# Performance work log

Measured on AMD Instinct MI355X. Metric: run time of the kernel, lower is better.

The kernel has to match this reference:

```python
import jax, jax.numpy as jnp
import numpy as np

N = 50000        # nodes
E = 800000       # edges (before self loops)
G = 512          # graphs
H = 2            # heads
FIN = 128        # in_features
CH = 64          # hidden per head
COUT = 32        # out_features
NEG_SLOPE = 0.2  # PyG GATConv default
BN_EPS = 1e-5


def _gat(x, src, dst, W, a_src, a_dst, b, concat, n):
    # x: [n, F], W: [F, H*C], a_src/a_dst: [H, C]
    h = (x @ W).reshape(n, a_src.shape[0], a_src.shape[1])        # [n, H, C]
    e = jax.nn.leaky_relu((h * a_src).sum(-1)[src]
                          + (h * a_dst).sum(-1)[dst], NEG_SLOPE)  # [Etot, H]
    # per-destination segment softmax (self loops guarantee nonempty segments)
    m = jax.ops.segment_max(e, dst, num_segments=n)
    ex = jnp.exp(e - m[dst])
    s = jax.ops.segment_sum(ex, dst, num_segments=n)
    alpha = ex / (s[dst] + 1e-16)                                 # [Etot, H]
    out = jax.ops.segment_sum(h[src] * alpha[:, :, None], dst, num_segments=n)
    out = out.reshape(n, -1) if concat else out.mean(axis=1)
    return out + b


def _bn(x, gamma, beta, mean, var):
    # BatchNorm1d in eval mode (running statistics)
    return (x - mean) * jax.lax.rsqrt(var + BN_EPS) * gamma + beta


def setup_inputs() -> dict:
    key = jax.random.key(0)
    ks = jax.random.split(key, 12)
    x = jax.random.normal(ks[0], (N, FIN), dtype=jnp.float32)
    edge_index = jax.random.randint(ks[1], (2, E), 0, N, dtype=jnp.int32)
    batch = jnp.sort(jax.random.randint(ks[2], (N,), 0, G, dtype=jnp.int32))
    inp = {"x": x, "edge_index": edge_index, "batch": batch}
    # layer 1: GATConv(FIN -> CH, heads=H, concat=True)
    inp["W1"] = jax.random.normal(ks[3], (FIN, H * CH), dtype=jnp.float32) * 0.1
    inp["as1"] = jax.random.normal(ks[4], (H, CH), dtype=jnp.float32) * 0.1
    inp["ad1"] = jax.random.normal(ks[5], (H, CH), dtype=jnp.float32) * 0.1
    inp["b1"] = jnp.zeros((H * CH,), dtype=jnp.float32)
    inp["bn1_gamma"] = jnp.ones((H * CH,), dtype=jnp.float32)
    inp["bn1_beta"] = jnp.zeros((H * CH,), dtype=jnp.float32)
    inp["bn1_mean"] = jax.random.normal(ks[6], (H * CH,), dtype=jnp.float32) * 0.05
    inp["bn1_var"] = jnp.ones((H * CH,), dtype=jnp.float32)
    # layer 2: GATConv(H*CH -> COUT, heads=H, concat=False)
    inp["W2"] = jax.random.normal(ks[7], (H * CH, H * COUT), dtype=jnp.float32) * 0.1
    inp["as2"] = jax.random.normal(ks[8], (H, COUT), dtype=jnp.float32) * 0.1
    inp["ad2"] = jax.random.normal(ks[9], (H, COUT), dtype=jnp.float32) * 0.1
    inp["b2"] = jnp.zeros((COUT,), dtype=jnp.float32)
    inp["bn2_gamma"] = jnp.ones((COUT,), dtype=jnp.float32)
    inp["bn2_beta"] = jnp.zeros((COUT,), dtype=jnp.float32)
    inp["bn2_mean"] = jax.random.normal(ks[10], (COUT,), dtype=jnp.float32) * 0.05
    inp["bn2_var"] = jnp.ones((COUT,), dtype=jnp.float32)
    return inp


def reference(x, edge_index, batch,
              W1, as1, ad1, b1, bn1_gamma, bn1_beta, bn1_mean, bn1_var,
              W2, as2, ad2, b2, bn2_gamma, bn2_beta, bn2_mean, bn2_var):
    n = x.shape[0]
    sl = jnp.arange(n, dtype=edge_index.dtype)
    src = jnp.concatenate([edge_index[0], sl])  # PyG add_self_loops=True
    dst = jnp.concatenate([edge_index[1], sl])
    h = _gat(x, src, dst, W1, as1, ad1, b1, True, n)
    h = jax.nn.relu(_bn(h, bn1_gamma, bn1_beta, bn1_mean, bn1_var))
    h = _gat(h, src, dst, W2, as2, ad2, b2, False, n)
    h = _bn(h, bn2_gamma, bn2_beta, bn2_mean, bn2_var)
    # global mean pool over graphs
    sums = jax.ops.segment_sum(h, batch, num_segments=G)
    cnts = jax.ops.segment_sum(jnp.ones((n,), h.dtype), batch, num_segments=G)
    pooled = sums / jnp.maximum(cnts, 1.0)[:, None]
    return jax.nn.log_softmax(pooled, axis=1)
```

## Files before the change

### kernel.cpp

```cpp
#include <hip/hip_runtime.h>
#include <hip/hip_bf16.h>

#define NEG_SLOPE 0.2f
#define BN_EPS 1e-5f
#define BSHIFT 7
#define P_PART 256
#define MAXB 512

typedef unsigned int uint32;
typedef unsigned short ushort16;
typedef __attribute__((ext_vector_type(8))) short bf16x8;
typedef __attribute__((ext_vector_type(4))) float f32x4;

__device__ __forceinline__ ushort16 f2bf(float f) {
    uint32 u = __float_as_uint(f);
    u = (u + 0x7fff + ((u >> 16) & 1)) >> 16;
    return (ushort16)u;
}
__device__ __forceinline__ float bfu_lo(uint32 u) { return __uint_as_float(u << 16); }
__device__ __forceinline__ float bfu_hi(uint32 u) { return __uint_as_float(u & 0xffff0000u); }

__global__ __launch_bounds__(256) void hist_part(const int* __restrict__ ei, int E, int Etot,
                                                 int nbuck, int chunk, int* __restrict__ hist) {
    const int p = blockIdx.x;
    __shared__ int lh[MAXB];
    for (int i = threadIdx.x; i < nbuck; i += 256) lh[i] = 0;
    __syncthreads();
    const int beg = p * chunk;
    const int end = min(beg + chunk, Etot);
    for (int i = beg + threadIdx.x; i < end; i += 256) {
        int d = (i < E) ? ei[E + i] : i - E;
        atomicAdd(&lh[d >> BSHIFT], 1);
    }
    __syncthreads();
    for (int i = threadIdx.x; i < nbuck; i += 256) hist[(size_t)i * P_PART + p] = lh[i];
}

__global__ __launch_bounds__(P_PART) void row_scan(int* __restrict__ hist,
                                                   int* __restrict__ rowtot) {
    const int b = blockIdx.x;
    __shared__ int s[P_PART];
    const int t = threadIdx.x;
    int v = hist[(size_t)b * P_PART + t];
    s[t] = v;
    __syncthreads();
    for (int off = 1; off < P_PART; off <<= 1) {
        int u = (t >= off) ? s[t - off] : 0;
        __syncthreads();
        s[t] += u;
        __syncthreads();
    }
    hist[(size_t)b * P_PART + t] = s[t] - v;
    if (t == P_PART - 1) rowtot[b] = s[t];
}

__global__ __launch_bounds__(512) void tot_scan(const int* __restrict__ rowtot,
                                                int* __restrict__ bbase, int nbuck, int Etot) {
    __shared__ int s[512];
    const int t = threadIdx.x;
    int v = (t < nbuck) ? rowtot[t] : 0;
    s[t] = v;
    __syncthreads();
    for (int off = 1; off < 512; off <<= 1) {
        int u = (t >= off) ? s[t - off] : 0;
        __syncthreads();
        s[t] += u;
        __syncthreads();
    }
    if (t < nbuck) bbase[t] = s[t] - v;
    if (t == 0) bbase[nbuck] = Etot;
}

__global__ __launch_bounds__(256) void rank_scatter(const int* __restrict__ ei, int E, int Etot,
                                                    int nbuck, int chunk,
                                                    const int* __restrict__ hist,
                                                    const int* __restrict__ bbase,
                                                    uint32* __restrict__ ebuf) {
    const int p = blockIdx.x;
    __shared__ int cur[MAXB];
    for (int i = threadIdx.x; i < nbuck; i += 256)
        cur[i] = bbase[i] + hist[(size_t)i * P_PART + p];
    __syncthreads();
    const int beg = p * chunk;
    const int end = min(beg + chunk, Etot);
    for (int i = beg + threadIdx.x; i < end; i += 256) {
        int s_, d_;
        if (i < E) { s_ = ei[i]; d_ = ei[E + i]; }
        else       { s_ = d_ = i - E; }
        int pos = atomicAdd(&cur[d_ >> BSHIFT], 1);
        ebuf[pos] = ((uint32)(d_ & ((1 << BSHIFT) - 1)) << 25) | (uint32)s_;
    }
}

__global__ __launch_bounds__(256) void bucket_place(
    const int* __restrict__ bbase, const uint32* __restrict__ ebuf, int N,
    int* __restrict__ base, int* __restrict__ csr_src) {
    const int bk = blockIdx.x;
    __shared__ int ldeg[1 << BSHIFT];
    __shared__ int sscan[1 << BSHIFT];
    __shared__ int lcur[1 << BSHIFT];
    const int t = threadIdx.x;
    if (t < (1 << BSHIFT)) { ldeg[t] = 0; lcur[t] = 0; }
    __syncthreads();
    const int beg = bbase[bk], end = bbase[bk + 1];
    for (int i = beg + t; i < end; i += 256) atomicAdd(&ldeg[ebuf[i] >> 25], 1);
    __syncthreads();
    if (t < 128) sscan[t] = ldeg[t];
    __syncthreads();
    for (int off = 1; off < 128; off <<= 1) {
        int v = 0;
        if (t < 128 && t >= off) v = sscan[t - off];
        __syncthreads();
        if (t < 128) sscan[t] += v;
        __syncthreads();
    }
    if (t < 128) {
        int node = (bk << BSHIFT) + t;
        if (node < N) base[node] = beg + sscan[t] - ldeg[t];
    }
    __syncthreads();
    for (int i = beg + t; i < end; i += 256) {
        uint32 pk = ebuf[i];
        int dl = (int)(pk >> 25);
        int s_ = (int)(pk & 0x1FFFFFFu);
        int pos = beg + (sscan[dl] - ldeg[dl]) + atomicAdd(&lcur[dl], 1);
        csr_src[pos] = s_;
    }
}

__global__ void graph_bounds(const int* __restrict__ batch, int N, int G,
                             int* __restrict__ gstart) {
    int g = blockIdx.x * blockDim.x + threadIdx.x;
    if (g > G) return;
    if (g == G) { gstart[G] = N; return; }
    int lo = 0, hi = N;
    while (lo < hi) { int mid = (lo + hi) >> 1; if (batch[mid] < g) lo = mid + 1; else hi = mid; }
    gstart[g] = lo;
}

template <int OC, int C>
__global__ void pack_w(const float* __restrict__ W, const float* __restrict__ a_s,
                       const float* __restrict__ a_d, ushort16* __restrict__ wt) {
    const int col = blockIdx.x;
    const int k = threadIdx.x;
    float v = 0.f;
    if (col < OC) {
        v = W[k * OC + col];
    } else if (col < OC + 2) {
        int hh = col - OC;
        float s = 0.f;
        for (int c = 0; c < C; ++c) s += W[k * OC + hh * C + c] * a_s[hh * C + c];
        v = s;
    } else if (col < OC + 4) {
        int hh = col - OC - 2;
        float s = 0.f;
        for (int c = 0; c < C; ++c) s += W[k * OC + hh * C + c] * a_d[hh * C + c];
        v = s;
    }
    wt[(size_t)col * 128 + k] = f2bf(v);
}

template <int OC, int NT, bool AF32>
__global__ __launch_bounds__(256) void gemm_mfma(
    const void* __restrict__ xin, const ushort16* __restrict__ wt,
    ushort16* __restrict__ h, float4* __restrict__ att, float2* __restrict__ asc, int N) {
    const int wave = threadIdx.x >> 6, lane = threadIdx.x & 63;
    const int tile = blockIdx.x * 4 + wave;
    if (tile * 16 >= N) return;
    const int m = lane & 15, quad = lane >> 4;
    const int node = tile * 16 + m;

    bf16x8 a[4];
    if (AF32) {
        const float* xr = (const float*)xin + (size_t)node * 128 + quad * 8;
#pragma unroll
        for (int c = 0; c < 4; ++c) {
            float4 u = *(const float4*)(xr + c * 32);
            float4 v = *(const float4*)(xr + c * 32 + 4);
            bf16x8 t;
            t[0] = (short)f2bf(u.x); t[1] = (short)f2bf(u.y);
            t[2] = (short)f2bf(u.z); t[3] = (short)f2bf(u.w);
            t[4] = (short)f2bf(v.x); t[5] = (short)f2bf(v.y);
            t[6] = (short)f2bf(v.z); t[7] = (short)f2bf(v.w);
            a[c] = t;
        }
    } else {
        const ushort16* xr = (const ushort16*)xin + (size_t)node * 128 + quad * 8;
#pragma unroll
        for (int c = 0; c < 4; ++c) a[c] = *(const bf16x8*)(xr + c * 32);
    }

    for (int t = 0; t < NT; ++t) {
        const ushort16* wr = wt + ((size_t)(t * 16 + m)) * 128 + quad * 8;
        bf16x8 b[4];
#pragma unroll
        for (int c = 0; c < 4; ++c) b[c] = *(const bf16x8*)(wr + c * 32);
        f32x4 acc = {0.f, 0.f, 0.f, 0.f};
#pragma unroll
        for (int c = 0; c < 4; ++c)
            acc = __builtin_amdgcn_mfma_f32_16x16x32_bf16(a[c], b[c], acc, 0, 0, 0);
        if (t * 16 < OC) {
#pragma unroll
            for (int r = 0; r < 4; ++r) {
                int nrow = tile * 16 + quad * 4 + r;
                h[(size_t)nrow * OC + t * 16 + m] = f2bf(acc[r]);
            }
        } else if (m < 4) {
#pragma unroll
            for (int r = 0; r < 4; ++r) {
                int nrow = tile * 16 + quad * 4 + r;
                ((float*)(att + nrow))[m] = acc[r];
                if (m < 2) ((float*)(asc + nrow))[m] = acc[r];
            }
        }
    }
}

__global__ __launch_bounds__(256) void gat_gather1(
    const int* __restrict__ base, const int* __restrict__ csr_src, int Etot, int N,
    const ushort16* __restrict__ h, const float4* __restrict__ att,
    const float2* __restrict__ asc,
    const float* __restrict__ b, const float* __restrict__ g, const float* __restrict__ be,
    const float* __restrict__ mu, const float* __restrict__ var,
    ushort16* __restrict__ outb) {
    const int node = __builtin_amdgcn_readfirstlane(blockIdx.x * 4 + (threadIdx.x >> 6));
    if (node >= N) return;
    const int t = threadIdx.x & 63;
    const int sub = t >> 4;
    const int q = t & 15;
    const int hh = q >> 3;
    const int beg = base[node];
    const int end = (node + 1 < N) ? base[node + 1] : Etot;
    const int deg = end - beg;
    const float4 adn = att[node];

    float a0 = 0.f, a1 = 0.f, a2 = 0.f, a3 = 0.f;
    float a4 = 0.f, a5 = 0.f, a6 = 0.f, a7 = 0.f;
    float ssum0 = 0.f, ssum1 = 0.f;

    for (int c0e = 0; c0e < deg; c0e += 64) {
        const int rel = c0e + t;
        const bool ok = rel < deg;
        const int sidxme = csr_src[beg + (ok ? rel : 0)];
        const float2 av = asc[sidxme];
        float e0 = av.x + adn.z, e1 = av.y + adn.w;
        e0 = e0 > 0.f ? e0 : NEG_SLOPE * e0;
        e1 = e1 > 0.f ? e1 : NEG_SLOPE * e1;
        const float x0 = ok ? __expf(e0) : 0.f;
        const float x1 = ok ? __expf(e1) : 0.f;
        float r0 = x0, r1 = x1;
#pragma unroll
        for (int off = 1; off < 64; off <<= 1) {
            r0 += __shfl_xor(r0, off, 64);
            r1 += __shfl_xor(r1, off, 64);
        }
        ssum0 += r0;
        ssum1 += r1;
        const int degc = min(deg - c0e, 64);
        const int kkmax = (degc + 3) >> 2;
        for (int kk = 0; kk < kkmax; kk += 4) {
            int sidx[4];
            float exv[4];
            uint4 hv[4];
#pragma unroll
            for (int j = 0; j < 4; ++j) {
                int sl = min(4 * (kk + j) + sub, 63);
                sidx[j] = __shfl(sidxme, sl, 64);
                float f0 = __shfl(x0, sl, 64);
                float f1 = __shfl(x1, sl, 64);
                exv[j] = hh ? f1 : f0;
                hv[j] = *(const uint4*)(h + (size_t)sidx[j] * 128 + 8 * q);
            }
#pragma unroll
            for (int j = 0; j < 4; ++j) {
                const float ex = exv[j];
                a0 += ex * bfu_lo(hv[j].x);
                a1 += ex * bfu_hi(hv[j].x);
                a2 += ex * bfu_lo(hv[j].y);
                a3 += ex * bfu_hi(hv[j].y);
                a4 += ex * bfu_lo(hv[j].z);
                a5 += ex * bfu_hi(hv[j].z);
                a6 += ex * bfu_lo(hv[j].w);
                a7 += ex * bfu_hi(hv[j].w);
            }
        }
    }
#pragma unroll
    for (int off = 16; off <= 32; off <<= 1) {
        a0 += __shfl_xor(a0, off, 64);
        a1 += __shfl_xor(a1, off, 64);
        a2 += __shfl_xor(a2, off, 64);
        a3 += __shfl_xor(a3, off, 64);
        a4 += __shfl_xor(a4, off, 64);
        a5 += __shfl_xor(a5, off, 64);
        a6 += __shfl_xor(a6, off, 64);
        a7 += __shfl_xor(a7, off, 64);
    }
    if (t < 16) {
        const float inv = 1.f / ((hh ? ssum1 : ssum0) + 1e-16f);
        const int c0 = 8 * q;
        float va[8] = {a0, a1, a2, a3, a4, a5, a6, a7};
        uint32 pk[4];
#pragma unroll
        for (int i = 0; i < 8; i += 2) {
            float v0 = va[i] * inv + b[c0 + i];
            float v1 = va[i + 1] * inv + b[c0 + i + 1];
            v0 = fmaxf((v0 - mu[c0 + i]) * rsqrtf(var[c0 + i] + BN_EPS) * g[c0 + i] + be[c0 + i], 0.f);
            v1 = fmaxf((v1 - mu[c0 + i + 1]) * rsqrtf(var[c0 + i + 1] + BN_EPS) * g[c0 + i + 1] + be[c0 + i + 1], 0.f);
            pk[i >> 1] = (uint32)f2bf(v0) | ((uint32)f2bf(v1) << 16);
        }
        uint4 r = make_uint4(pk[0], pk[1], pk[2], pk[3]);
        *(uint4*)(outb + (size_t)node * 128 + c0) = r;
    }
}

__global__ __launch_bounds__(256) void gat_gather2(
    const int* __restrict__ base, const int* __restrict__ csr_src, int Etot, int N,
    const ushort16* __restrict__ h2, const float4* __restrict__ att,
    const float2* __restrict__ asc,
    const float* __restrict__ b2, const float* __restrict__ g, const float* __restrict__ be,
    const float* __restrict__ mu, const float* __restrict__ var,
    float* __restrict__ node_out) {
    const int node = __builtin_amdgcn_readfirstlane(blockIdx.x * 4 + (threadIdx.x >> 6));
    if (node >= N) return;
    const int t = threadIdx.x & 63;
    const int sub = t >> 4;
    const int q = t & 15;
    const int hh = q >> 3;
    const int beg = base[node];
    const int end = (node + 1 < N) ? base[node + 1] : Etot;
    const int deg = end - beg;
    const float4 adn = att[node];

    float a0 = 0.f, a1 = 0.f, a2 = 0.f, a3 = 0.f;
    float ssum0 = 0.f, ssum1 = 0.f;

    for (int c0e = 0; c0e < deg; c0e += 64) {
        const int rel = c0e + t;
        const bool ok = rel < deg;
        const int sidxme = csr_src[beg + (ok ? rel : 0)];
        const float2 av = asc[sidxme];
        float e0 = av.x + adn.z, e1 = av.y + adn.w;
        e0 = e0 > 0.f ? e0 : NEG_SLOPE * e0;
        e1 = e1 > 0.f ? e1 : NEG_SLOPE * e1;
        const float x0 = ok ? __expf(e0) : 0.f;
        const float x1 = ok ? __expf(e1) : 0.f;
        float r0 = x0, r1 = x1;
#pragma unroll
        for (int off = 1; off < 64; off <<= 1) {
            r0 += __shfl_xor(r0, off, 64);
            r1 += __shfl_xor(r1, off, 64);
        }
        ssum0 += r0;
        ssum1 += r1;
        const int degc = min(deg - c0e, 64);
        const int kkmax = (degc + 3) >> 2;
        for (int kk = 0; kk < kkmax; kk += 4) {
            int sidx[4];
            float exv[4];
            uint2 hv[4];
#pragma unroll
            for (int j = 0; j < 4; ++j) {
                int sl = min(4 * (kk + j) + sub, 63);
                sidx[j] = __shfl(sidxme, sl, 64);
                float f0 = __shfl(x0, sl, 64);
                float f1 = __shfl(x1, sl, 64);
                exv[j] = hh ? f1 : f0;
                hv[j] = *(const uint2*)(h2 + (size_t)sidx[j] * 64 + 4 * q);
            }
#pragma unroll
            for (int j = 0; j < 4; ++j) {
                const float ex = exv[j];
                a0 += ex * bfu_lo(hv[j].x);
                a1 += ex * bfu_hi(hv[j].x);
                a2 += ex * bfu_lo(hv[j].y);
                a3 += ex * bfu_hi(hv[j].y);
            }
        }
    }
#pragma unroll
    for (int off = 16; off <= 32; off <<= 1) {
        a0 += __shfl_xor(a0, off, 64);
        a1 += __shfl_xor(a1, off, 64);
        a2 += __shfl_xor(a2, off, 64);
        a3 += __shfl_xor(a3, off, 64);
    }
    const float inv = 1.f / ((hh ? ssum1 : ssum0) + 1e-16f);
    float v0 = a0 * inv, v1 = a1 * inv, v2 = a2 * inv, v3 = a3 * inv;
    const int src = (t & 15) + 8;
    float p0 = __shfl(v0, src, 64);
    float p1 = __shfl(v1, src, 64);
    float p2 = __shfl(v2, src, 64);
    float p3 = __shfl(v3, src, 64);
    if (t < 8) {
        const int c0 = 4 * t;
        float m0 = 0.5f * (v0 + p0) + b2[c0];
        float m1 = 0.5f * (v1 + p1) + b2[c0 + 1];
        float m2 = 0.5f * (v2 + p2) + b2[c0 + 2];
        float m3 = 0.5f * (v3 + p3) + b2[c0 + 3];
        m0 = (m0 - mu[c0]) * rsqrtf(var[c0] + BN_EPS) * g[c0] + be[c0];
        m1 = (m1 - mu[c0 + 1]) * rsqrtf(var[c0 + 1] + BN_EPS) * g[c0 + 1] + be[c0 + 1];
        m2 = (m2 - mu[c0 + 2]) * rsqrtf(var[c0 + 2] + BN_EPS) * g[c0 + 2] + be[c0 + 2];
        m3 = (m3 - mu[c0 + 3]) * rsqrtf(var[c0 + 3] + BN_EPS) * g[c0 + 3] + be[c0 + 3];
        *(float4*)(node_out + (size_t)node * 32 + c0) = make_float4(m0, m1, m2, m3);
    }
}

__global__ __launch_bounds__(256) void pool_logsoftmax(
    const float* __restrict__ node_out, const int* __restrict__ gstart,
    float* __restrict__ out) {
    const int gidx = blockIdx.x;
    const int tid = threadIdx.x;
    const int c = tid & 31, r = tid >> 5;
    const int n0 = gstart[gidx], n1 = gstart[gidx + 1];
    float s = 0.f;
    for (int n = n0 + r; n < n1; n += 8) s += node_out[(size_t)n * 32 + c];
    __shared__ float red[8][32];
    red[r][c] = s;
    __syncthreads();
    if (r == 0) {
        float tot = red[0][c];
#pragma unroll
        for (int k = 1; k < 8; ++k) tot += red[k][c];
        float v = tot / fmaxf((float)(n1 - n0), 1.f);
        float m = v;
#pragma unroll
        for (int off = 16; off >= 1; off >>= 1) m = fmaxf(m, __shfl_xor(m, off, 64));
        float ex = __expf(v - m);
        float ssum = ex;
#pragma unroll
        for (int off = 16; off >= 1; off >>= 1) ssum += __shfl_xor(ssum, off, 64);
        out[gidx * 32 + c] = v - m - logf(ssum);
    }
}

extern "C" void kernel_launch(void* const* d_in, const int* in_sizes, int n_in,
                              void* d_out, int out_size, void* d_ws, size_t ws_size,
                              hipStream_t stream) {
    const float* x   = (const float*)d_in[0];
    const int* ei    = (const int*)d_in[1];
    const int* batch = (const int*)d_in[2];
    const float* W1  = (const float*)d_in[3];
    const float* as1 = (const float*)d_in[4];
    const float* ad1 = (const float*)d_in[5];
    const float* b1  = (const float*)d_in[6];
    const float* g1  = (const float*)d_in[7];
    const float* be1 = (const float*)d_in[8];
    const float* mu1 = (const float*)d_in[9];
    const float* vr1 = (const float*)d_in[10];
    const float* W2  = (const float*)d_in[11];
    const float* as2 = (const float*)d_in[12];
    const float* ad2 = (const float*)d_in[13];
    const float* b2  = (const float*)d_in[14];
    const float* g2  = (const float*)d_in[15];
    const float* be2 = (const float*)d_in[16];
    const float* mu2 = (const float*)d_in[17];
    const float* vr2 = (const float*)d_in[18];
    float* out = (float*)d_out;

    const int N = in_sizes[0] / 128;
    const int E = in_sizes[1] / 2;
    const int Etot = E + N;
    const int G = out_size / 32;
    const int nbuck = (N + (1 << BSHIFT) - 1) >> BSHIFT;
    const int chunk = (Etot + P_PART - 1) / P_PART;
    const int M = nbuck * P_PART;
    const int ntile = (N + 15) / 16;
    const int gemm_grid = (ntile + 3) / 4;

    float* p = (float*)d_ws;
    size_t o = 0;
    auto al = [&]() { o = (o + 3) & ~(size_t)3; };
    ushort16* h1b   = (ushort16*)(p + o); o += (size_t)N * 64;  al();
    ushort16* agg1b = (ushort16*)(p + o); o += (size_t)N * 64;  al();
    ushort16* h2b   = (ushort16*)(p + o); o += (size_t)N * 32;  al();
    float4* att1 = (float4*)(p + o); o += (size_t)N * 4;  al();
    float4* att2 = (float4*)(p + o); o += (size_t)N * 4;  al();
    float2* asc1 = (float2*)(p + o); o += (size_t)N * 2;  al();
    float2* asc2 = (float2*)(p + o); o += (size_t)N * 2;  al();
    float* nodeo = p + o; o += (size_t)N * 32; al();
    ushort16* wt1 = (ushort16*)(p + o); o += (size_t)144 * 64; al();
    ushort16* wt2 = (ushort16*)(p + o); o += (size_t)80 * 64;  al();
    int* csr_src = (int*)(p + o); o += (size_t)Etot; al();
    uint32* ebuf = (uint32*)(p + o); o += (size_t)Etot; al();
    int* base    = (int*)(p + o); o += (size_t)N;    al();
    int* hist    = (int*)(p + o); o += (size_t)M;    al();
    int* rowtot  = (int*)(p + o); o += (size_t)nbuck + 4; al();
    int* bbase   = (int*)(p + o); o += (size_t)nbuck + 4; al();
    int* gstart  = (int*)(p + o); o += (size_t)G + 4; al();

    hist_part<<<P_PART, 256, 0, stream>>>(ei, E, Etot, nbuck, chunk, hist);
    row_scan<<<nbuck, P_PART, 0, stream>>>(hist, rowtot);
    tot_scan<<<1, 512, 0, stream>>>(rowtot, bbase, nbuck, Etot);
    rank_scatter<<<P_PART, 256, 0, stream>>>(ei, E, Etot, nbuck, chunk, hist, bbase, ebuf);
    bucket_place<<<nbuck, 256, 0, stream>>>(bbase, ebuf, N, base, csr_src);
    graph_bounds<<<(G + 256) / 256, 256, 0, stream>>>(batch, N, G, gstart);
    pack_w<128, 64><<<144, 128, 0, stream>>>(W1, as1, ad1, wt1);
    pack_w<64, 32><<<80, 128, 0, stream>>>(W2, as2, ad2, wt2);

    gemm_mfma<128, 9, true><<<gemm_grid, 256, 0, stream>>>(x, wt1, h1b, att1, asc1, N);
    gat_gather1<<<(N + 3) / 4, 256, 0, stream>>>(base, csr_src, Etot, N, h1b, att1, asc1,
                                                 b1, g1, be1, mu1, vr1, agg1b);
    gemm_mfma<64, 5, false><<<gemm_grid, 256, 0, stream>>>(agg1b, wt2, h2b, att2, asc2, N);
    gat_gather2<<<(N + 3) / 4, 256, 0, stream>>>(base, csr_src, Etot, N, h2b, att2, asc2,
                                                 b2, g2, be2, mu2, vr2, nodeo);

    pool_logsoftmax<<<G, 256, 0, stream>>>(nodeo, gstart, out);
}
```

Measured before the change: 246.7 us.

## Fuse independent prep kernels and overlap GEMM1 with edge scatter

Merges the histogram, weight packing and graph-bound search into one launch using block-index ranges. The separate total-scan kernel is removed: each block of the scatter and bucket-place kernels recomputes the bucket base scan redundantly in shared memory. The layer-1 GEMM now runs in the same launch as the rank scatter, so the two independent stages can overlap. Launch count drops from 13 to 8, in exchange for redundant scan work per block and higher shared-memory use.

```diff
diff --git a/kernel.cpp b/kernel.cpp
--- a/kernel.cpp
+++ b/kernel.cpp
@@ -20,129 +20,35 @@
 __device__ __forceinline__ float bfu_lo(uint32 u) { return __uint_as_float(u << 16); }
 __device__ __forceinline__ float bfu_hi(uint32 u) { return __uint_as_float(u & 0xffff0000u); }
 
-__global__ __launch_bounds__(256) void hist_part(const int* __restrict__ ei, int E, int Etot,
-                                                 int nbuck, int chunk, int* __restrict__ hist) {
-    const int p = blockIdx.x;
-    __shared__ int lh[MAXB];
-    for (int i = threadIdx.x; i < nbuck; i += 256) lh[i] = 0;
-    __syncthreads();
-    const int beg = p * chunk;
-    const int end = min(beg + chunk, Etot);
-    for (int i = beg + threadIdx.x; i < end; i += 256) {
-        int d = (i < E) ? ei[E + i] : i - E;
-        atomicAdd(&lh[d >> BSHIFT], 1);
-    }
-    __syncthreads();
-    for (int i = threadIdx.x; i < nbuck; i += 256) hist[(size_t)i * P_PART + p] = lh[i];
-}
-
-__global__ __launch_bounds__(P_PART) void row_scan(int* __restrict__ hist,
-                                                   int* __restrict__ rowtot) {
-    const int b = blockIdx.x;
-    __shared__ int s[P_PART];
+__device__ __forceinline__ void scan_bbase(const int* __restrict__ rowtot, int nbuck,
+                                           int Etot, int* sb ) {
     const int t = threadIdx.x;
-    int v = hist[(size_t)b * P_PART + t];
-    s[t] = v;
-    __syncthreads();
-    for (int off = 1; off < P_PART; off <<= 1) {
-        int u = (t >= off) ? s[t - off] : 0;
-        __syncthreads();
-        s[t] += u;
-        __syncthreads();
-    }
-    hist[(size_t)b * P_PART + t] = s[t] - v;
-    if (t == P_PART - 1) rowtot[b] = s[t];
-}
-
-__global__ __launch_bounds__(512) void tot_scan(const int* __restrict__ rowtot,
-                                                int* __restrict__ bbase, int nbuck, int Etot) {
-    __shared__ int s[512];
-    const int t = threadIdx.x;
-    int v = (t < nbuck) ? rowtot[t] : 0;
-    s[t] = v;
+    int v0 = (t < nbuck) ? rowtot[t] : 0;
+    int v1 = (256 + t < nbuck) ? rowtot[256 + t] : 0;
+    sb[t] = v0;
+    sb[256 + t] = v1;
     __syncthreads();
     for (int off = 1; off < 512; off <<= 1) {
-        int u = (t >= off) ? s[t - off] : 0;
-        __syncthreads();
-        s[t] += u;
-        __syncthreads();
-    }
-    if (t < nbuck) bbase[t] = s[t] - v;
-    if (t == 0) bbase[nbuck] = Etot;
-}
-
-__global__ __launch_bounds__(256) void rank_scatter(const int* __restrict__ ei, int E, int Etot,
-                                                    int nbuck, int chunk,
-                                                    const int* __restrict__ hist,
-                                                    const int* __restrict__ bbase,
-                                                    uint32* __restrict__ ebuf) {
-    const int p = blockIdx.x;
-    __shared__ int cur[MAXB];
-    for (int i = threadIdx.x; i < nbuck; i += 256)
-        cur[i] = bbase[i] + hist[(size_t)i * P_PART + p];
-    __syncthreads();
-    const int beg = p * chunk;
-    const int end = min(beg + chunk, Etot);
-    for (int i = beg + threadIdx.x; i < end; i += 256) {
-        int s_, d_;
-        if (i < E) { s_ = ei[i]; d_ = ei[E + i]; }
-        else       { s_ = d_ = i - E; }
-        int pos = atomicAdd(&cur[d_ >> BSHIFT], 1);
-        ebuf[pos] = ((uint32)(d_ & ((1 << BSHIFT) - 1)) << 25) | (uint32)s_;
-    }
-}
-
-__global__ __launch_bounds__(256) void bucket_place(
-    const int* __restrict__ bbase, const uint32* __restrict__ ebuf, int N,
-    int* __restrict__ base, int* __restrict__ csr_src) {
-    const int bk = blockIdx.x;
-    __shared__ int ldeg[1 << BSHIFT];
-    __shared__ int sscan[1 << BSHIFT];
-    __shared__ int lcur[1 << BSHIFT];
-    const int t = threadIdx.x;
-    if (t < (1 << BSHIFT)) { ldeg[t] = 0; lcur[t] = 0; }
-    __syncthreads();
-    const int beg = bbase[bk], end = bbase[bk + 1];
-    for (int i = beg + t; i < end; i += 256) atomicAdd(&ldeg[ebuf[i] >> 25], 1);
-    __syncthreads();
-    if (t < 128) sscan[t] = ldeg[t];
-    __syncthreads();
-    for (int off = 1; off < 128; off <<= 1) {
-        int v = 0;
-        if (t < 128 && t >= off) v = sscan[t - off];
-        __syncthreads();
-        if (t < 128) sscan[t] += v;
-        __syncthreads();
-    }
-    if (t < 128) {
-        int node = (bk << BSHIFT) + t;
-        if (node < N) base[node] = beg + sscan[t] - ldeg[t];
-    }
-    __syncthreads();
-    for (int i = beg + t; i < end; i += 256) {
-        uint32 pk = ebuf[i];
-        int dl = (int)(pk >> 25);
-        int s_ = (int)(pk & 0x1FFFFFFu);
-        int pos = beg + (sscan[dl] - ldeg[dl]) + atomicAdd(&lcur[dl], 1);
-        csr_src[pos] = s_;
-    }
-}
-
-__global__ void graph_bounds(const int* __restrict__ batch, int N, int G,
-                             int* __restrict__ gstart) {
-    int g = blockIdx.x * blockDim.x + threadIdx.x;
-    if (g > G) return;
-    if (g == G) { gstart[G] = N; return; }
-    int lo = 0, hi = N;
-    while (lo < hi) { int mid = (lo + hi) >> 1; if (batch[mid] < g) lo = mid + 1; else hi = mid; }
-    gstart[g] = lo;
+        int a0 = (t >= off) ? sb[t - off] : 0;
+        int a1 = (256 + t >= off) ? sb[256 + t - off] : 0;
+        __syncthreads();
+        sb[t] += a0;
+        sb[256 + t] += a1;
+        __syncthreads();
+    }
+    int i0 = sb[t], i1 = sb[256 + t];
+    __syncthreads();
+    sb[t] = i0 - v0;
+    sb[256 + t] = i1 - v1;
+    if (t == 0) sb[MAXB] = Etot;
+    __syncthreads();
 }
 
 template <int OC, int C>
-__global__ void pack_w(const float* __restrict__ W, const float* __restrict__ a_s,
-                       const float* __restrict__ a_d, ushort16* __restrict__ wt) {
-    const int col = blockIdx.x;
-    const int k = threadIdx.x;
+__device__ __forceinline__ void pack_col(int col, int k, const float* __restrict__ W,
+                                         const float* __restrict__ a_s,
+                                         const float* __restrict__ a_d,
+                                         ushort16* __restrict__ wt) {
     float v = 0.f;
     if (col < OC) {
         v = W[k * OC + col];
@@ -161,11 +67,12 @@
 }
 
 template <int OC, int NT, bool AF32>
-__global__ __launch_bounds__(256) void gemm_mfma(
-    const void* __restrict__ xin, const ushort16* __restrict__ wt,
-    ushort16* __restrict__ h, float4* __restrict__ att, float2* __restrict__ asc, int N) {
+__device__ __forceinline__ void gemm_body(int gb, const void* __restrict__ xin,
+                                          const ushort16* __restrict__ wt,
+                                          ushort16* __restrict__ h, float4* __restrict__ att,
+                                          float2* __restrict__ asc, int N) {
     const int wave = threadIdx.x >> 6, lane = threadIdx.x & 63;
-    const int tile = blockIdx.x * 4 + wave;
+    const int tile = gb * 4 + wave;
     if (tile * 16 >= N) return;
     const int m = lane & 15, quad = lane >> 4;
     const int node = tile * 16 + m;
@@ -214,6 +121,140 @@
             }
         }
     }
+}
+
+__global__ __launch_bounds__(256) void fused_prep(
+    const int* __restrict__ ei, int E, int Etot, int nbuck, int chunk, int* __restrict__ hist,
+    const float* __restrict__ W1, const float* __restrict__ as1, const float* __restrict__ ad1,
+    ushort16* __restrict__ wt1,
+    const float* __restrict__ W2, const float* __restrict__ as2, const float* __restrict__ ad2,
+    ushort16* __restrict__ wt2,
+    const int* __restrict__ batch, int N, int G, int* __restrict__ gstart) {
+    const int bid = blockIdx.x;
+    if (bid < P_PART) {
+        __shared__ int lh[MAXB];
+        const int p = bid;
+        for (int i = threadIdx.x; i < nbuck; i += 256) lh[i] = 0;
+        __syncthreads();
+        const int beg = p * chunk;
+        const int end = min(beg + chunk, Etot);
+        for (int i = beg + threadIdx.x; i < end; i += 256) {
+            int d = (i < E) ? ei[E + i] : i - E;
+            atomicAdd(&lh[d >> BSHIFT], 1);
+        }
+        __syncthreads();
+        for (int i = threadIdx.x; i < nbuck; i += 256) hist[(size_t)i * P_PART + p] = lh[i];
+        return;
+    }
+    int rb = bid - P_PART;
+    if (rb < 72) {
+        pack_col<128, 64>(rb * 2 + (threadIdx.x >> 7), threadIdx.x & 127, W1, as1, ad1, wt1);
+        return;
+    }
+    rb -= 72;
+    if (rb < 40) {
+        pack_col<64, 32>(rb * 2 + (threadIdx.x >> 7), threadIdx.x & 127, W2, as2, ad2, wt2);
+        return;
+    }
+    rb -= 40;
+    {
+        int g = rb * 256 + (int)threadIdx.x;
+        if (g > G) return;
+        if (g == G) { gstart[G] = N; return; }
+        int lo = 0, hi = N;
+        while (lo < hi) { int mid = (lo + hi) >> 1; if (batch[mid] < g) lo = mid + 1; else hi = mid; }
+        gstart[g] = lo;
+    }
+}
+
+__global__ __launch_bounds__(P_PART) void row_scan(int* __restrict__ hist,
+                                                   int* __restrict__ rowtot) {
+    const int b = blockIdx.x;
+    __shared__ int s[P_PART];
+    const int t = threadIdx.x;
+    int v = hist[(size_t)b * P_PART + t];
+    s[t] = v;
+    __syncthreads();
+    for (int off = 1; off < P_PART; off <<= 1) {
+        int u = (t >= off) ? s[t - off] : 0;
+        __syncthreads();
+        s[t] += u;
+        __syncthreads();
+    }
+    hist[(size_t)b * P_PART + t] = s[t] - v;
+    if (t == P_PART - 1) rowtot[b] = s[t];
+}
+
+__global__ __launch_bounds__(256) void fused_scatter_gemm1(
+    const int* __restrict__ ei, int E, int Etot, int nbuck, int chunk,
+    const int* __restrict__ hist, const int* __restrict__ rowtot, uint32* __restrict__ ebuf,
+    const void* __restrict__ x, const ushort16* __restrict__ wt1,
+    ushort16* __restrict__ h1, float4* __restrict__ att1, float2* __restrict__ asc1, int N) {
+    const int bid = blockIdx.x;
+    if (bid < P_PART) {
+        __shared__ int sb[MAXB + 1];
+        __shared__ int cur[MAXB];
+        scan_bbase(rowtot, nbuck, Etot, sb);
+        const int p = bid;
+        for (int i = threadIdx.x; i < nbuck; i += 256)
+            cur[i] = sb[i] + hist[(size_t)i * P_PART + p];
+        __syncthreads();
+        const int beg = p * chunk;
+        const int end = min(beg + chunk, Etot);
+        for (int i = beg + threadIdx.x; i < end; i += 256) {
+            int s_, d_;
+            if (i < E) { s_ = ei[i]; d_ = ei[E + i]; }
+            else       { s_ = d_ = i - E; }
+            int pos = atomicAdd(&cur[d_ >> BSHIFT], 1);
+            ebuf[pos] = ((uint32)(d_ & ((1 << BSHIFT) - 1)) << 25) | (uint32)s_;
+        }
+    } else {
+        gemm_body<128, 9, true>(bid - P_PART, x, wt1, h1, att1, asc1, N);
+    }
+}
+
+__global__ __launch_bounds__(256) void bucket_place(
+    const int* __restrict__ rowtot, int nbuck, int Etot, const uint32* __restrict__ ebuf,
+    int N, int* __restrict__ base, int* __restrict__ csr_src) {
+    const int bk = blockIdx.x;
+    __shared__ int sb[MAXB + 1];
+    __shared__ int ldeg[1 << BSHIFT];
+    __shared__ int sscan[1 << BSHIFT];
+    __shared__ int lcur[1 << BSHIFT];
+    scan_bbase(rowtot, nbuck, Etot, sb);
+    const int t = threadIdx.x;
+    if (t < (1 << BSHIFT)) { ldeg[t] = 0; lcur[t] = 0; }
+    __syncthreads();
+    const int beg = sb[bk], end = sb[bk + 1];
+    for (int i = beg + t; i < end; i += 256) atomicAdd(&ldeg[ebuf[i] >> 25], 1);
+    __syncthreads();
+    if (t < 128) sscan[t] = ldeg[t];
+    __syncthreads();
+    for (int off = 1; off < 128; off <<= 1) {
+        int v = 0;
+        if (t < 128 && t >= off) v = sscan[t - off];
+        __syncthreads();
+        if (t < 128) sscan[t] += v;
+        __syncthreads();
+    }
+    if (t < 128) {
+        int node = (bk << BSHIFT) + t;
+        if (node < N) base[node] = beg + sscan[t] - ldeg[t];
+    }
+    __syncthreads();
+    for (int i = beg + t; i < end; i += 256) {
+        uint32 pk = ebuf[i];
+        int dl = (int)(pk >> 25);
+        int s_ = (int)(pk & 0x1FFFFFFu);
+        int pos = beg + (sscan[dl] - ldeg[dl]) + atomicAdd(&lcur[dl], 1);
+        csr_src[pos] = s_;
+    }
+}
+
+__global__ __launch_bounds__(256) void gemm2_kernel(
+    const void* __restrict__ xin, const ushort16* __restrict__ wt,
+    ushort16* __restrict__ h, float4* __restrict__ att, float2* __restrict__ asc, int N) {
+    gemm_body<64, 5, false>(blockIdx.x, xin, wt, h, att, asc, N);
 }
 
 __global__ __launch_bounds__(256) void gat_gather1(
@@ -467,6 +508,7 @@
     const int M = nbuck * P_PART;
     const int ntile = (N + 15) / 16;
     const int gemm_grid = (ntile + 3) / 4;
+    const int gbb = (G + 1 + 255) / 256;
 
     float* p = (float*)d_ws;
     size_t o = 0;
@@ -486,24 +528,19 @@
     int* base    = (int*)(p + o); o += (size_t)N;    al();
     int* hist    = (int*)(p + o); o += (size_t)M;    al();
     int* rowtot  = (int*)(p + o); o += (size_t)nbuck + 4; al();
-    int* bbase   = (int*)(p + o); o += (size_t)nbuck + 4; al();
     int* gstart  = (int*)(p + o); o += (size_t)G + 4; al();
 
-    hist_part<<<P_PART, 256, 0, stream>>>(ei, E, Etot, nbuck, chunk, hist);
+    fused_prep<<<P_PART + 72 + 40 + gbb, 256, 0, stream>>>(
+        ei, E, Etot, nbuck, chunk, hist, W1, as1, ad1, wt1, W2, as2, ad2, wt2,
+        batch, N, G, gstart);
     row_scan<<<nbuck, P_PART, 0, stream>>>(hist, rowtot);
-    tot_scan<<<1, 512, 0, stream>>>(rowtot, bbase, nbuck, Etot);
-    rank_scatter<<<P_PART, 256, 0, stream>>>(ei, E, Etot, nbuck, chunk, hist, bbase, ebuf);
-    bucket_place<<<nbuck, 256, 0, stream>>>(bbase, ebuf, N, base, csr_src);
-    graph_bounds<<<(G + 256) / 256, 256, 0, stream>>>(batch, N, G, gstart);
-    pack_w<128, 64><<<144, 128, 0, stream>>>(W1, as1, ad1, wt1);
-    pack_w<64, 32><<<80, 128, 0, stream>>>(W2, as2, ad2, wt2);
-
-    gemm_mfma<128, 9, true><<<gemm_grid, 256, 0, stream>>>(x, wt1, h1b, att1, asc1, N);
+    fused_scatter_gemm1<<<P_PART + gemm_grid, 256, 0, stream>>>(
+        ei, E, Etot, nbuck, chunk, hist, rowtot, ebuf, x, wt1, h1b, att1, asc1, N);
+    bucket_place<<<nbuck, 256, 0, stream>>>(rowtot, nbuck, Etot, ebuf, N, base, csr_src);
     gat_gather1<<<(N + 3) / 4, 256, 0, stream>>>(base, csr_src, Etot, N, h1b, att1, asc1,
                                                  b1, g1, be1, mu1, vr1, agg1b);
-    gemm_mfma<64, 5, false><<<gemm_grid, 256, 0, stream>>>(agg1b, wt2, h2b, att2, asc2, N);
+    gemm2_kernel<<<gemm_grid, 256, 0, stream>>>(agg1b, wt2, h2b, att2, asc2, N);
     gat_gather2<<<(N + 3) / 4, 256, 0, stream>>>(base, csr_src, Etot, N, h2b, att2, asc2,
                                                  b2, g2, be2, mu2, vr2, nodeo);
-
     pool_logsoftmax<<<G, 256, 0, stream>>>(nodeo, gstart, out);
 }
```

Measured after the change: 234.4 us. 1.05x faster.
